# Performance work log

Hardware: AMD Instinct MI355X
Metric: run time of the kernel (lower is better)

The kernel has to match this reference:

```python
import jax, jax.numpy as jnp
import numpy as np

B, S, D, H, DFF = 2, 4096, 512, 8, 2048
DK = D // H
EPS = 1e-5


def layer_norm(x, g, b):
    mu = jnp.mean(x, axis=-1, keepdims=True)
    var = jnp.mean((x - mu) ** 2, axis=-1, keepdims=True)
    return (x - mu) * jax.lax.rsqrt(var + EPS) * g + b


def setup_inputs() -> dict:
    key = jax.random.key(0)
    ks = jax.random.split(key, 12)
    s = 1.0 / np.sqrt(D)
    return {
        "x": jax.random.normal(ks[0], (B, S, D), jnp.float32),
        "mask": jnp.ones((B, 1, 1, S), jnp.int32),
        "wq": jax.random.normal(ks[1], (D, D), jnp.float32) * s,
        "wk": jax.random.normal(ks[2], (D, D), jnp.float32) * s,
        "wv": jax.random.normal(ks[3], (D, D), jnp.float32) * s,
        "wo": jax.random.normal(ks[4], (D, D), jnp.float32) * s,
        "w1": jax.random.normal(ks[5], (D, DFF), jnp.float32) * s,
        "b1": jnp.zeros((DFF,), jnp.float32),
        "w2": jax.random.normal(ks[6], (DFF, D), jnp.float32) * (1.0 / np.sqrt(DFF)),
        "b2": jnp.zeros((D,), jnp.float32),
        "g1": jnp.ones((D,), jnp.float32),
        "be1": jnp.zeros((D,), jnp.float32),
        "g2": jnp.ones((D,), jnp.float32),
        "be2": jnp.zeros((D,), jnp.float32),
    }


def reference(x, mask, wq, wk, wv, wo, w1, b1, w2, b2, g1, be1, g2, be2):
    # projections -> [B, H, S, DK]
    def split_heads(t):
        return t.reshape(B, S, H, DK).transpose(0, 2, 1, 3)

    q = split_heads(x @ wq)
    k = split_heads(x @ wk)
    v = split_heads(x @ wv)

    scores = jnp.einsum("bhqd,bhkd->bhqk", q, k) / np.sqrt(DK)
    scores = jnp.where(mask == 0, -1e9, scores)
    attn = jax.nn.softmax(scores, axis=-1)  # dropout=0 (eval)
    ctx = jnp.einsum("bhqk,bhkd->bhqd", attn, v)
    ctx = ctx.transpose(0, 2, 1, 3).reshape(B, S, D)
    attn_out = ctx @ wo

    x1 = layer_norm(x + attn_out, g1, be1)
    ff = jax.nn.relu(x1 @ w1 + b1) @ w2 + b2
    return layer_norm(x1 + ff, g2, be2)
```

## Files before the change

### kernel.cpp

```cpp
#include <hip/hip_runtime.h>
#include <hip/hip_bf16.h>


typedef unsigned short u16;
typedef unsigned int u32;
typedef __attribute__((ext_vector_type(2))) u32 u32x2;
typedef __attribute__((ext_vector_type(4))) u16 u16x4;
typedef __attribute__((ext_vector_type(8))) u16 u16x8;
typedef __attribute__((ext_vector_type(2))) float f32x2;
typedef __attribute__((ext_vector_type(4))) float f32x4;
typedef __attribute__((ext_vector_type(16))) float f32x16;
typedef __attribute__((ext_vector_type(8))) short bf16x8;

#define CB 2
#define CS 4096
#define CD 512
#define CH 8
#define CDK 64
#define CDFF 2048
#define NXC ((size_t)CB * CS * CD)
#define NSP 2
#define BH (CB * CH)
#define BHS (BH * CS)

__device__ __forceinline__ float bf2f(u16 u) {
    union { u32 i; float f; } c;
    c.i = ((u32)u) << 16;
    return c.f;
}

__device__ __forceinline__ u16 f2bf(float f) {
    u32 x = __float_as_uint(f);
    u32 r = (x + 0x7fffu + ((x >> 16) & 1u)) >> 16;
    return (u16)r;
}

__device__ __forceinline__ u32 packbf2(float a, float b) {
    __hip_bfloat162 h = __float22bfloat162_rn(float2{a, b});
    union { __hip_bfloat162 h; u32 u; } c;
    c.h = h;
    return c.u;
}

__device__ __forceinline__ void dma16(const u16* g, u16* l) {
    __builtin_amdgcn_global_load_lds(
        (const __attribute__((address_space(1))) void*)g,
        (__attribute__((address_space(3))) void*)l, 16, 0, 0);
}

__global__ void detect_dtype(const u32* __restrict__ xw, int* __restrict__ flag) {
    __shared__ int red[256];
    int sane = 0;
    for (int i = threadIdx.x; i < 2048; i += 256) {
        u32 w = xw[i];
        u32 lo = w & 0xFFFFu;
        u32 e = (lo >> 7) & 0xFFu;
        if (lo == 0u || lo == 0x8000u || (e >= 96u && e <= 159u)) sane++;
    }
    red[threadIdx.x] = sane;
    __syncthreads();
    for (int s = 128; s > 0; s >>= 1) {
        if ((int)threadIdx.x < s) red[threadIdx.x] += red[threadIdx.x + s];
        __syncthreads();
    }
    if (threadIdx.x == 0) *flag = (red[0] >= 1843) ? 1 : 0;
}

__global__ __launch_bounds__(256) void convert_bf16(
    const void* __restrict__ src, u16* __restrict__ dst, int n,
    const int* __restrict__ flag)
{
    const bool isbf = (*flag != 0);
    const int n8 = n >> 3;
    int i = blockIdx.x * 256 + threadIdx.x;
    const int stride = gridDim.x * 256;
    if (isbf) {
        const u16x8* s = (const u16x8*)src;
        u16x8* d = (u16x8*)dst;
        for (; i < n8; i += stride) d[i] = s[i];
    } else {
        const f32x4* s = (const f32x4*)src;
        for (; i < n8; i += stride) {
            f32x4 a = s[2 * i];
            f32x4 b = s[2 * i + 1];
            u16x8 o;
#pragma unroll
            for (int e = 0; e < 4; e++) {
                o[e] = f2bf(a[e]);
                o[4 + e] = f2bf(b[e]);
            }
            *(u16x8*)&dst[(size_t)i * 8] = o;
        }
    }
    if (blockIdx.x == 0 && threadIdx.x == 0) {
        for (int r = n8 * 8; r < n; r++) {
            if (isbf) dst[r] = ((const u16*)src)[r];
            else dst[r] = f2bf(((const float*)src)[r]);
        }
    }
}

struct SmallConv {
    const void* src[6];
    u16* dst[6];
    int n[6];
};

__global__ __launch_bounds__(256) void convert_small(SmallConv sc, const int* __restrict__ flag) {
    const bool isbf = (*flag != 0);
    for (int t = 0; t < 6; t++) {
        for (int i = threadIdx.x; i < sc.n[t]; i += 256) {
            if (isbf) sc.dst[t][i] = ((const u16*)sc.src[t])[i];
            else sc.dst[t][i] = f2bf(((const float*)sc.src[t])[i]);
        }
    }
}

__global__ __launch_bounds__(256) void build_mask_bits(
    const int* __restrict__ mask, unsigned long long* __restrict__ bits)
{
    int w = blockIdx.x * 4 + (threadIdx.x >> 6);
    int lane = threadIdx.x & 63;
    int b = w >> 6, t = w & 63;
    int val = mask[b * CS + t * 64 + lane];
    unsigned long long bal = __ballot(val != 0);
    if (lane == 0) bits[w] = bal;
}

__global__ __launch_bounds__(256) void transpose_cvt(
    const void* __restrict__ src, u16* __restrict__ dst,
    int R, int Cc, const int* __restrict__ flag)
{
    __shared__ float t[32][33];
    const bool isbf = (*flag != 0);
    const int r0 = blockIdx.y * 32;
    const int c0 = blockIdx.x * 32;
    const int col = threadIdx.x & 31;
    const int row = threadIdx.x >> 5;
#pragma unroll
    for (int it = 0; it < 4; it++) {
        int rr = row + it * 8;
        float v;
        if (isbf) v = bf2f(((const u16*)src)[(size_t)(r0 + rr) * Cc + c0 + col]);
        else v = ((const float*)src)[(size_t)(r0 + rr) * Cc + c0 + col];
        t[rr][col] = v;
    }
    __syncthreads();
#pragma unroll
    for (int it = 0; it < 4; it++) {
        int rr = row + it * 8;
        dst[(size_t)(c0 + rr) * R + r0 + col] = f2bf(t[col][rr]);
    }
}

#define F_SPLIT 1
#define F_BIAS  2
#define F_RELU  4

template <int FLAGS>
__global__ __launch_bounds__(256, 2) void gemm_mfma(
    const u16* __restrict__ A, const u16* __restrict__ Bt,
    const u16* __restrict__ bias, u16* __restrict__ C,
    int M, int N, int K)
{
    __shared__ u16 Asb[4096];
    __shared__ u16 Bsb[4096];

    const int tid = threadIdx.x;
    const int lane = tid & 63;
    const int wave = tid >> 6;
    const int lrow = lane & 15;
    const int quad = lane >> 4;
    const int wm = wave & 1;
    const int wn = wave >> 1;
    const int m0 = blockIdx.y * 128;
    const int n0 = blockIdx.x * 128;

    const int idx0 = wave * 128 + lane;
    const int idx1 = idx0 + 64;
    const u16* Ap0 = A + (size_t)(m0 + (idx0 >> 2)) * K + (idx0 & 3) * 8;
    const u16* Ap1 = A + (size_t)(m0 + (idx1 >> 2)) * K + (idx1 & 3) * 8;
    const u16* Bp0 = Bt + (size_t)(n0 + (idx0 >> 2)) * K + (idx0 & 3) * 8;
    const u16* Bp1 = Bt + (size_t)(n0 + (idx1 >> 2)) * K + (idx1 & 3) * 8;
    u16* Al0 = &Asb[wave * 1024];
    u16* Al1 = &Asb[wave * 1024 + 512];
    u16* Bl0 = &Bsb[wave * 1024];
    u16* Bl1 = &Bsb[wave * 1024 + 512];

    f32x4 acc[4][4];
#pragma unroll
    for (int i = 0; i < 4; i++)
#pragma unroll
        for (int j = 0; j < 4; j++) acc[i][j] = f32x4{0.f, 0.f, 0.f, 0.f};

    for (int k0 = 0; k0 < K; k0 += 32) {
        __syncthreads();
        dma16(Ap0 + k0, Al0);
        dma16(Ap1 + k0, Al1);
        dma16(Bp0 + k0, Bl0);
        dma16(Bp1 + k0, Bl1);
        __syncthreads();

        bf16x8 af[4], bfr[4];
#pragma unroll
        for (int i = 0; i < 4; i++)
            af[i] = *(const bf16x8*)&Asb[(wm * 64 + i * 16 + lrow) * 32 + quad * 8];
#pragma unroll
        for (int j = 0; j < 4; j++)
            bfr[j] = *(const bf16x8*)&Bsb[(wn * 64 + j * 16 + lrow) * 32 + quad * 8];
#pragma unroll
        for (int i = 0; i < 4; i++)
#pragma unroll
            for (int j = 0; j < 4; j++)
                acc[i][j] = __builtin_amdgcn_mfma_f32_16x16x32_bf16(
                    af[i], bfr[j], acc[i][j], 0, 0, 0);
    }

    const int mbase = m0 + wm * 64;
    const int nbase = n0 + wn * 64;
#pragma unroll
    for (int i = 0; i < 4; i++) {
#pragma unroll
        for (int j = 0; j < 4; j++) {
            const int n = nbase + j * 16 + lrow;
            if ((FLAGS & F_SPLIT) && ((nbase + j * 16) >> 9) == 2) {
                const int dk = n & 63;
                const int h = (n >> 6) & 7;
                const int sb = mbase + i * 16 + quad * 4;
                const int bb = sb >> 12;
                const int ss = sb & 4095;
                u16x4 ov;
#pragma unroll
                for (int r = 0; r < 4; r++) ov[r] = f2bf(acc[i][j][r]);
                *(u16x4*)&C[2 * NXC + (((size_t)(bb * CH + h)) * CDK + dk) * CS + ss] = ov;
            } else {
#pragma unroll
                for (int r = 0; r < 4; r++) {
                    const int m = mbase + i * 16 + quad * 4 + r;
                    float val = acc[i][j][r];
                    if (FLAGS & F_BIAS) val += bf2f(bias[n]);
                    if (FLAGS & F_RELU) val = fmaxf(val, 0.f);
                    if (FLAGS & F_SPLIT) {
                        const int proj = n >> 9;
                        const int d = n & 511;
                        const int h = d >> 6;
                        const int dk = d & 63;
                        const int bb = m >> 12;
                        const int ss = m & 4095;
                        C[proj * NXC + (((size_t)(bb * CH + h)) * CS + ss) * CDK + dk] = f2bf(val);
                    } else {
                        C[(size_t)m * N + n] = f2bf(val);
                    }
                }
            }
        }
    }
}

__global__ __launch_bounds__(256, 4) void mfma_attn2(
    const u16* __restrict__ Qb, const u16* __restrict__ Kb,
    const u16* __restrict__ Vt, const unsigned long long* __restrict__ bits,
    u16* __restrict__ pOT, float* __restrict__ Ls)
{
    __shared__ u16 KB[3][4096];
    __shared__ u16 VB[2][4096];

    const int tid = threadIdx.x;
    const int lane = tid & 63;
    const int wave = tid >> 6;
    const int qcol = lane & 31;
    const int hf = lane >> 5;

    const int bh = blockIdx.y;
    const int b = bh >> 3;
    const int z = blockIdx.z;
    const int q0 = blockIdx.x * 128 + wave * 32;

    const float SC = 0.125f * 1.44269504088896340736f;

    bf16x8 bq[4];
    const u16* qp = Qb + ((size_t)bh * CS + q0 + qcol) * CDK + hf * 8;
#pragma unroll
    for (int c = 0; c < 4; c++) {
        bf16x8 raw = *(const bf16x8*)(qp + c * 16);
        union { u32 u[4]; bf16x8 v; } cv;
#pragma unroll
        for (int j = 0; j < 4; j++)
            cv.u[j] = packbf2(bf2f((u16)raw[2 * j]) * SC, bf2f((u16)raw[2 * j + 1]) * SC);
        bq[c] = cv.v;
    }

    f32x4 z4 = {0.f, 0.f, 0.f, 0.f};
    asm volatile("" : "+v"(z4));
    f32x16 zero16;
#pragma unroll
    for (int i = 0; i < 16; i++) zero16[i] = z4[i & 3];

    f32x16 ot[2];
#pragma unroll
    for (int dt = 0; dt < 2; dt++)
#pragma unroll
        for (int i = 0; i < 16; i++) ot[dt][i] = 0.f;
    float l = 0.f;

    const u16* kbase = Kb + (size_t)bh * CS * CDK;
    const u16* vbase = Vt + (size_t)bh * CDK * CS;
    const unsigned long long* bp = bits + b * 64;

    const int t0 = z * (CS / NSP);
    const int t1 = t0 + (CS / NSP);

    const int rsw = qcol & 7;
    int koff[2][4];
#pragma unroll
    for (int rt = 0; rt < 2; rt++)
#pragma unroll
        for (int c = 0; c < 4; c++)
            koff[rt][c] = ((rt * 32 + qcol) * 64 + (((2 * c + hf) ^ rsw) * 8)) * 2;
    const char* kb0 = (const char*)&KB[0][0];
    const char* vb0 = (const char*)&VB[0][0];

    const int w2 = wave * 2;

#define STAGE_K(KOFFB, t)                                                    \
    {                                                                        \
        const u16* kb_ = kbase + (size_t)(t) * CDK;                          \
        _Pragma("unroll")                                                    \
        for (int n = 0; n < 2; n++) {                                        \
            int idx = (w2 + n) * 64 + lane;                                  \
            int row = idx >> 3;                                              \
            int g = (idx & 7) ^ (row & 7);                                   \
            dma16(kb_ + row * CDK + g * 8,                                   \
                  (u16*)((char*)&KB[0][0] + (KOFFB) + (w2 + n) * 1024));     \
        }                                                                    \
    }
#define STAGE_V(P, t)                                                        \
    {                                                                        \
        const u16* vb_ = vbase + (t);                                        \
        _Pragma("unroll")                                                    \
        for (int n = 0; n < 2; n++) {                                        \
            int idx = (w2 + n) * 64 + lane;                                  \
            int row = idx >> 3;                                              \
            int g = (idx & 7) ^ (row & 7);                                   \
            dma16(vb_ + (size_t)row * CS + g * 8,                            \
                  (u16*)((char*)&VB[0][0] + (P) * 8192 + (w2 + n) * 1024));  \
        }                                                                    \
    }

#define TBODY(KROFF, VOFF, BM, MASKED, MIDSYNC)                              \
    {                                                                        \
        f32x2 racc = {0.f, 0.f};                                             \
        _Pragma("unroll")                                                    \
        for (int mt = 0; mt < 2; mt++) {                                     \
            f32x16 s;                                                        \
            _Pragma("unroll")                                                \
            for (int c = 0; c < 4; c++) {                                    \
                bf16x8 ak = *(const bf16x8*)(kb0 + (KROFF) + koff[mt][c]);   \
                s = __builtin_amdgcn_mfma_f32_32x32x16_bf16(                 \
                    ak, bq[c], (c == 0) ? zero16 : s, 0, 0, 0);              \
            }                                                                \
            if (MASKED) {                                                    \
                const unsigned long long bm_ = (BM);                         \
                if (bm_ != ~0ull) {                                          \
                    _Pragma("unroll")                                        \
                    for (int i = 0; i < 16; i++) {                           \
                        const int key = (i & 3) + 8 * (i >> 2) + 4 * hf + 32 * mt; \
                        if (!((bm_ >> key) & 1ull)) s[i] = -1e30f;           \
                    }                                                        \
                }                                                            \
            }                                                                \
            u32 pk[8];                                                       \
            _Pragma("unroll")                                                \
            for (int g = 0; g < 4; g++) {                                    \
                float p0 = __builtin_amdgcn_exp2f(s[4 * g + 0]);             \
                float p1 = __builtin_amdgcn_exp2f(s[4 * g + 1]);             \
                float p2 = __builtin_amdgcn_exp2f(s[4 * g + 2]);             \
                float p3 = __builtin_amdgcn_exp2f(s[4 * g + 3]);             \
                racc += f32x2{p0, p1};                                       \
                racc += f32x2{p2, p3};                                       \
                pk[2 * g + 0] = packbf2(p0, p1);                             \
                pk[2 * g + 1] = packbf2(p2, p3);                             \
            }                                                                \
            if (mt == 0) { MIDSYNC }                                         \
            _Pragma("unroll")                                                \
            for (int cc = 0; cc < 2; cc++) {                                 \
                u32x2 r0 = __builtin_amdgcn_permlane32_swap(                 \
                    pk[4 * cc + 0], pk[4 * cc + 2], false, false);           \
                u32x2 r1 = __builtin_amdgcn_permlane32_swap(                 \
                    pk[4 * cc + 1], pk[4 * cc + 3], false, false);           \
                union { u32 u[4]; bf16x8 v; } pf;                            \
                pf.u[0] = r0.x;                                              \
                pf.u[1] = r1.x;                                              \
                pf.u[2] = r0.y;                                              \
                pf.u[3] = r1.y;                                              \
                const int c = 2 * mt + cc;                                   \
                _Pragma("unroll")                                            \
                for (int dt = 0; dt < 2; dt++) {                             \
                    bf16x8 av = *(const bf16x8*)(vb0 + (VOFF) + koff[dt][c]); \
                    ot[dt] = __builtin_amdgcn_mfma_f32_32x32x16_bf16(        \
                        av, pf.v, ot[dt], 0, 0, 0);                          \
                }                                                            \
            }                                                                \
        }                                                                    \
        float rsv = racc.x + racc.y;                                         \
        u32x2 rr = __builtin_amdgcn_permlane32_swap(                         \
            __float_as_uint(rsv), __float_as_uint(rsv), false, false);       \
        l += rsv + __uint_as_float(hf ? rr.x : rr.y);                        \
    }

#define FTILE(P, TT, KR, KS, DOV, DOK, TOPASM, MIDASM)                       \
    {                                                                        \
        asm volatile(TOPASM ::: "memory");                                   \
        __builtin_amdgcn_sched_barrier(0);                                   \
        __builtin_amdgcn_s_barrier();                                        \
        __builtin_amdgcn_sched_barrier(0);                                   \
        if (DOV) STAGE_V((P) ^ 1, (TT) + 64);                                \
        if (DOK) STAGE_K((KS), (TT) + 128);                                  \
        TBODY((KR), (P) * 8192, 0ull, 0,                                     \
              asm volatile(MIDASM ::: "memory");                             \
              __builtin_amdgcn_sched_barrier(0);                             \
              __builtin_amdgcn_s_barrier();                                  \
              __builtin_amdgcn_sched_barrier(0);)                            \
    }

    unsigned long long am = ~0ull;
    const int tb0 = t0 >> 6;
    for (int i = 0; i < 32; i++) am &= bp[tb0 + i];
    const bool allones = (am == ~0ull);

    if (allones) {
        STAGE_K(0, t0);
        STAGE_V(0, t0);
        STAGE_K(8192, t0 + 64);

        u32 kr = 0;
        for (int m = 0; m < 15; m++) {
            const int t = t0 + m * 128;
            const u32 kr1 = (kr == 16384u) ? 0u : kr + 8192u;
            const u32 ks0 = (kr1 == 16384u) ? 0u : kr1 + 8192u;
            FTILE(0, t, kr, ks0, 1, 1,
                  "s_waitcnt vmcnt(4)", "s_waitcnt vmcnt(6)")
            FTILE(1, t + 64, kr1, kr, 1, 1,
                  "s_waitcnt vmcnt(4)", "s_waitcnt vmcnt(6)")
            kr = ks0;
        }
        {
            const int t = t0 + 30 * 64;
            const u32 kr1 = (kr == 16384u) ? 0u : kr + 8192u;
            FTILE(0, t, kr, 0, 1, 0,
                  "s_waitcnt vmcnt(4)", "s_waitcnt vmcnt(4)")
            FTILE(1, t + 64, kr1, 0, 0, 0,
                  "s_waitcnt vmcnt(2)", "s_waitcnt vmcnt(0)")
        }
    } else {
        STAGE_K(0, t0);
        STAGE_V(0, t0);
        __syncthreads();
        for (int t = t0; t < t1; t += 64) {
            const int p = (t >> 6) & 1;
            const u32 kro = (u32)p * 8192u;
            if (t + 64 < t1) {
                STAGE_V(p ^ 1, t + 64);
                STAGE_K((p ^ 1) * 8192, t + 64);
            }
            TBODY(kro, p * 8192, bp[t >> 6], 1, ;)
            __syncthreads();
        }
    }
#undef FTILE
#undef TBODY
#undef STAGE_V
#undef STAGE_K

    const int q_lin = bh * CS + q0 + qcol;
    if (hf == 0) Ls[z * BHS + q_lin] = l;
    const size_t pbase = ((size_t)(z * BH + bh) * CDK) * CS + q0 + qcol;
#pragma unroll
    for (int dt = 0; dt < 2; dt++)
#pragma unroll
        for (int i = 0; i < 16; i++) {
            const int dk = (i & 3) + 8 * (i >> 2) + 4 * hf + 32 * dt;
            pOT[pbase + (size_t)dk * CS] = f2bf(ot[dt][i]);
        }
}

__global__ __launch_bounds__(256) void attn_combine(
    const u16* __restrict__ pOT, const float* __restrict__ Ls,
    u16* __restrict__ ctx)
{
    __shared__ float linv[64];
    __shared__ u16 T[64][72];

    const int bh = blockIdx.y;
    const int s0 = blockIdx.x * 64;
    const int b = bh >> 3, h = bh & 7;
    const int tid = threadIdx.x;

    if (tid < 64) {
        float L = 0.f;
#pragma unroll
        for (int z = 0; z < NSP; z++) L += Ls[z * BHS + bh * CS + s0 + tid];
        linv[tid] = (L > 0.f) ? 1.f / L : 0.f;
    }
    __syncthreads();

    const int dk = tid >> 2;
    const int sc = (tid & 3) * 16;
    float acc[16] = {};
#pragma unroll
    for (int z = 0; z < NSP; z++) {
        const u16* p = pOT + ((size_t)(z * BH + bh) * CDK + dk) * CS + s0 + sc;
        u16x8 v0 = *(const u16x8*)p;
        u16x8 v1 = *(const u16x8*)(p + 8);
#pragma unroll
        for (int e = 0; e < 8; e++) {
            acc[e] += bf2f(v0[e]);
            acc[8 + e] += bf2f(v1[e]);
        }
    }
#pragma unroll
    for (int e = 0; e < 16; e++)
        T[sc + e][dk] = f2bf(acc[e] * linv[sc + e]);
    __syncthreads();

    const int sr = tid >> 2;
    const int dc = (tid & 3) * 16;
    u16x8 o0, o1;
#pragma unroll
    for (int e = 0; e < 8; e++) {
        o0[e] = T[sr][dc + e];
        o1[e] = T[sr][dc + 8 + e];
    }
    u16* cp = &ctx[((size_t)b * CS + s0 + sr) * CD + h * CDK + dc];
    *(u16x8*)cp = o0;
    *(u16x8*)(cp + 8) = o1;
}

__global__ __launch_bounds__(256) void ln_kernel(
    const u16* __restrict__ xa, const u16* __restrict__ xb,
    const u16* __restrict__ g, const u16* __restrict__ be,
    u16* __restrict__ outb, float* __restrict__ outf,
    const int* __restrict__ flag)
{
    const int lane = threadIdx.x & 63;
    const int wave = threadIdx.x >> 6;
    const size_t row = (size_t)blockIdx.x * 4 + wave;
    const int c0 = lane * 8;

    u16x8 av = *(const u16x8*)(xa + row * CD + c0);
    u16x8 bv = *(const u16x8*)(xb + row * CD + c0);

    float v[8];
    float s1 = 0.f, s2 = 0.f;
#pragma unroll
    for (int e = 0; e < 8; e++) {
        v[e] = bf2f(av[e]) + bf2f(bv[e]);
        s1 += v[e];
        s2 += v[e] * v[e];
    }
#pragma unroll
    for (int off = 32; off > 0; off >>= 1) {
        s1 += __shfl_xor(s1, off, 64);
        s2 += __shfl_xor(s2, off, 64);
    }
    const float mu = s1 * (1.f / CD);
    const float var = fmaxf(s2 * (1.f / CD) - mu * mu, 0.f);
    const float r = rsqrtf(var + 1e-5f);

    u16x8 gv = *(const u16x8*)(g + c0);
    u16x8 ev = *(const u16x8*)(be + c0);
    float res[8];
#pragma unroll
    for (int e = 0; e < 8; e++)
        res[e] = (v[e] - mu) * r * bf2f(gv[e]) + bf2f(ev[e]);

    const int flg = *flag;
    const bool f32out = (outf != nullptr) && (flg == 0);
    if (f32out) {
        float4 o0 = make_float4(res[0], res[1], res[2], res[3]);
        float4 o1 = make_float4(res[4], res[5], res[6], res[7]);
        *(float4*)(outf + row * CD + c0) = o0;
        *(float4*)(outf + row * CD + c0 + 4) = o1;
    } else {
        u16x8 ov;
#pragma unroll
        for (int e = 0; e < 8; e++) ov[e] = f2bf(res[e]);
        *(u16x8*)(outb + row * CD + c0) = ov;
    }
}


extern "C" void kernel_launch(void* const* d_in, const int* in_sizes, int n_in,
                              void* d_out, int out_size, void* d_ws, size_t ws_size,
                              hipStream_t stream)
{
    const void* x_raw   = d_in[0];
    const int*  mask    = (const int*)d_in[1];
    const void* wq_raw  = d_in[2];
    const void* wk_raw  = d_in[3];
    const void* wv_raw  = d_in[4];
    const void* wo_raw  = d_in[5];
    const void* w1_raw  = d_in[6];
    const void* b1_raw  = d_in[7];
    const void* w2_raw  = d_in[8];
    const void* b2_raw  = d_in[9];
    const void* g1_raw  = d_in[10];
    const void* be1_raw = d_in[11];
    const void* g2_raw  = d_in[12];
    const void* be2_raw = d_in[13];

    const size_t NX = NXC;
    const size_t WSZ = (size_t)CD * CD;
    const size_t W1SZ = (size_t)CD * CDFF;

    u16* ws = (u16*)d_ws;
    int* flag = (int*)d_ws;
    unsigned long long* bits = (unsigned long long*)(ws + 512);
    u16* base = ws + 1024;
    u16* xc  = base;
    u16* q   = base + 1 * NX;
    u16* k   = base + 2 * NX;
    u16* v   = base + 3 * NX;
    u16* ctx = base + 4 * NX;
    u16* att = base + 5 * NX;
    u16* x1  = base + 6 * NX;
    u16* ffo = base + 7 * NX;
    u16* ffh = base + 8 * NX;
    u16* wt  = base + 12 * NX;
    u16* wqkvT = wt;
    u16* woT = wqkvT + 3 * WSZ;
    u16* w1T = woT + WSZ;
    u16* w2T = w1T + W1SZ;
    u16* b1c = w2T + W1SZ;
    u16* b2c = b1c + CDFF;
    u16* g1c = b2c + CD;
    u16* be1c = g1c + CD;
    u16* g2c = be1c + CD;
    u16* be2c = g2c + CD;
    u16* wend = be2c + CD;

    const size_t need = (size_t)(wend - ws) * sizeof(u16);
    if (ws_size < need) return;
    (void)k;

    u16* pOT = ffh;
    float* Ls = (float*)att;

    detect_dtype<<<1, 256, 0, stream>>>((const u32*)x_raw, flag);

    convert_bf16<<<1024, 256, 0, stream>>>(x_raw, xc, (int)NX, flag);
    build_mask_bits<<<32, 256, 0, stream>>>(mask, bits);

    transpose_cvt<<<dim3(CD / 32, CD / 32), 256, 0, stream>>>(wq_raw, wqkvT, CD, CD, flag);
    transpose_cvt<<<dim3(CD / 32, CD / 32), 256, 0, stream>>>(wk_raw, wqkvT + WSZ, CD, CD, flag);
    transpose_cvt<<<dim3(CD / 32, CD / 32), 256, 0, stream>>>(wv_raw, wqkvT + 2 * WSZ, CD, CD, flag);
    transpose_cvt<<<dim3(CD / 32, CD / 32), 256, 0, stream>>>(wo_raw, woT, CD, CD, flag);
    transpose_cvt<<<dim3(CDFF / 32, CD / 32), 256, 0, stream>>>(w1_raw, w1T, CD, CDFF, flag);
    transpose_cvt<<<dim3(CD / 32, CDFF / 32), 256, 0, stream>>>(w2_raw, w2T, CDFF, CD, flag);

    SmallConv sc;
    sc.src[0] = b1_raw;  sc.dst[0] = b1c;  sc.n[0] = CDFF;
    sc.src[1] = b2_raw;  sc.dst[1] = b2c;  sc.n[1] = CD;
    sc.src[2] = g1_raw;  sc.dst[2] = g1c;  sc.n[2] = CD;
    sc.src[3] = be1_raw; sc.dst[3] = be1c; sc.n[3] = CD;
    sc.src[4] = g2_raw;  sc.dst[4] = g2c;  sc.n[4] = CD;
    sc.src[5] = be2_raw; sc.dst[5] = be2c; sc.n[5] = CD;
    convert_small<<<1, 256, 0, stream>>>(sc, flag);

    const int M = CB * CS;

    gemm_mfma<F_SPLIT><<<dim3(1536 / 128, M / 128), 256, 0, stream>>>(
        xc, wqkvT, nullptr, q, M, 1536, CD);

    mfma_attn2<<<dim3(CS / 128, BH, NSP), 256, 0, stream>>>(q, k, v, bits, pOT, Ls);
    attn_combine<<<dim3(CS / 64, BH), 256, 0, stream>>>(pOT, Ls, ctx);

    gemm_mfma<0><<<dim3(CD / 128, M / 128), 256, 0, stream>>>(
        ctx, woT, nullptr, att, M, CD, CD);

    ln_kernel<<<dim3(M / 4), 256, 0, stream>>>(xc, att, g1c, be1c, x1, nullptr, flag);

    gemm_mfma<F_BIAS | F_RELU><<<dim3(CDFF / 128, M / 128), 256, 0, stream>>>(
        x1, w1T, b1c, ffh, M, CDFF, CD);
    gemm_mfma<F_BIAS><<<dim3(CD / 128, M / 128), 256, 0, stream>>>(
        ffh, w2T, b2c, ffo, M, CD, CDFF);

    ln_kernel<<<dim3(M / 4), 256, 0, stream>>>(x1, ffo, g2c, be2c,
                                               (u16*)d_out, (float*)d_out, flag);
}
```

Before: 339.9 us.

## Drop mid-tile barrier, unroll K ring by six, defer row-sum lane swap

Removes the second workgroup barrier and its vmcnt wait inside each attention tile, leaving one barrier per tile. The fast path is unrolled six tiles deep so the three-slot K ring and two-slot V ring offsets become compile-time constants, replacing the runtime modulo arithmetic. The per-tile permlane32 swap used for the softmax row sum is moved to a single swap after the loop. Taking out the mid-tile barrier relies on the remaining top barrier and wait count being enough to protect the K and V buffers from being overwritten while still in use, so there is some risk of a race on shared memory.

```diff
diff --git a/kernel.cpp b/kernel.cpp
--- a/kernel.cpp
+++ b/kernel.cpp
@@ -301,7 +301,7 @@
     for (int dt = 0; dt < 2; dt++)
 #pragma unroll
         for (int i = 0; i < 16; i++) ot[dt][i] = 0.f;
-    float l = 0.f;
+    float lh = 0.f;
 
     const u16* kbase = Kb + (size_t)bh * CS * CDK;
     const u16* vbase = Vt + (size_t)bh * CDK * CS;
@@ -347,7 +347,7 @@
         }                                                                    \
     }
 
-#define TBODY(KROFF, VOFF, BM, MASKED, MIDSYNC)                              \
+#define TBODY(KROFF, VOFF, BM, MASKED)                                       \
     {                                                                        \
         f32x2 racc = {0.f, 0.f};                                             \
         _Pragma("unroll")                                                    \
@@ -381,7 +381,6 @@
                 pk[2 * g + 0] = packbf2(p0, p1);                             \
                 pk[2 * g + 1] = packbf2(p2, p3);                             \
             }                                                                \
-            if (mt == 0) { MIDSYNC }                                         \
             _Pragma("unroll")                                                \
             for (int cc = 0; cc < 2; cc++) {                                 \
                 u32x2 r0 = __builtin_amdgcn_permlane32_swap(                 \
@@ -402,25 +401,18 @@
                 }                                                            \
             }                                                                \
         }                                                                    \
-        float rsv = racc.x + racc.y;                                         \
-        u32x2 rr = __builtin_amdgcn_permlane32_swap(                         \
-            __float_as_uint(rsv), __float_as_uint(rsv), false, false);       \
-        l += rsv + __uint_as_float(hf ? rr.x : rr.y);                        \
-    }
-
-#define FTILE(P, TT, KR, KS, DOV, DOK, TOPASM, MIDASM)                       \
+        lh += racc.x + racc.y;                                               \
+    }
+
+#define FTILE(P, KR, TT, DOV, DOK, KS, WAITASM)                              \
     {                                                                        \
-        asm volatile(TOPASM ::: "memory");                                   \
+        asm volatile(WAITASM ::: "memory");                                  \
         __builtin_amdgcn_sched_barrier(0);                                   \
         __builtin_amdgcn_s_barrier();                                        \
         __builtin_amdgcn_sched_barrier(0);                                   \
         if (DOV) STAGE_V((P) ^ 1, (TT) + 64);                                \
         if (DOK) STAGE_K((KS), (TT) + 128);                                  \
-        TBODY((KR), (P) * 8192, 0ull, 0,                                     \
-              asm volatile(MIDASM ::: "memory");                             \
-              __builtin_amdgcn_sched_barrier(0);                             \
-              __builtin_amdgcn_s_barrier();                                  \
-              __builtin_amdgcn_sched_barrier(0);)                            \
+        TBODY((KR), (P) * 8192, 0ull, 0)                                     \
     }
 
     unsigned long long am = ~0ull;
@@ -433,25 +425,17 @@
         STAGE_V(0, t0);
         STAGE_K(8192, t0 + 64);
 
-        u32 kr = 0;
-        for (int m = 0; m < 15; m++) {
-            const int t = t0 + m * 128;
-            const u32 kr1 = (kr == 16384u) ? 0u : kr + 8192u;
-            const u32 ks0 = (kr1 == 16384u) ? 0u : kr1 + 8192u;
-            FTILE(0, t, kr, ks0, 1, 1,
-                  "s_waitcnt vmcnt(4)", "s_waitcnt vmcnt(6)")
-            FTILE(1, t + 64, kr1, kr, 1, 1,
-                  "s_waitcnt vmcnt(4)", "s_waitcnt vmcnt(6)")
-            kr = ks0;
-        }
-        {
-            const int t = t0 + 30 * 64;
-            const u32 kr1 = (kr == 16384u) ? 0u : kr + 8192u;
-            FTILE(0, t, kr, 0, 1, 0,
-                  "s_waitcnt vmcnt(4)", "s_waitcnt vmcnt(4)")
-            FTILE(1, t + 64, kr1, 0, 0, 0,
-                  "s_waitcnt vmcnt(2)", "s_waitcnt vmcnt(0)")
-        }
+        for (int m = 0; m < 5; m++) {
+            const int t = t0 + m * 384;
+            FTILE(0, 0,     t,       1, 1, 16384, "s_waitcnt vmcnt(2)")
+            FTILE(1, 8192,  t + 64,  1, 1, 0,     "s_waitcnt vmcnt(2)")
+            FTILE(0, 16384, t + 128, 1, 1, 8192,  "s_waitcnt vmcnt(2)")
+            FTILE(1, 0,     t + 192, 1, 1, 16384, "s_waitcnt vmcnt(2)")
+            FTILE(0, 8192,  t + 256, 1, 1, 0,     "s_waitcnt vmcnt(2)")
+            FTILE(1, 16384, t + 320, 1, 1, 8192,  "s_waitcnt vmcnt(2)")
+        }
+        FTILE(0, 0, t0 + 1920, 1, 0, 0, "s_waitcnt vmcnt(2)")
+        FTILE(1, 8192, t0 + 1984, 0, 0, 0, "s_waitcnt vmcnt(0)")
     } else {
         STAGE_K(0, t0);
         STAGE_V(0, t0);
@@ -463,7 +447,7 @@
                 STAGE_V(p ^ 1, t + 64);
                 STAGE_K((p ^ 1) * 8192, t + 64);
             }
-            TBODY(kro, p * 8192, bp[t >> 6], 1, ;)
+            TBODY(kro, p * 8192, bp[t >> 6], 1)
             __syncthreads();
         }
     }
@@ -471,6 +455,10 @@
 #undef TBODY
 #undef STAGE_V
 #undef STAGE_K
+
+    u32x2 rr = __builtin_amdgcn_permlane32_swap(
+        __float_as_uint(lh), __float_as_uint(lh), false, false);
+    const float l = lh + __uint_as_float(hf ? rr.x : rr.y);
 
     const int q_lin = bh * CS + q0 + qcol;
     if (hf == 0) Ls[z * BHS + q_lin] = l;
```

After: 353.3 us. 3.9% more time.

## Triple-buffer GEMM LDS staging and defer attention row-sum lane swap

Applied to the files above, without the earlier changes.

The bf16 MFMA GEMM now keeps three LDS buffers and issues asynchronous global-to-LDS loads two k-steps ahead. Each step uses an explicit vmcnt wait and a single barrier, replacing the two full barriers per k-step that left load latency exposed. A fallback loop handles K values that do not fit the unrolled schedule. In the attention kernel, the per-tile permlane32 swap for the softmax row sum is moved out of the loop and done once at the end. The cost is triple the GEMM shared memory (48KB), which may reduce occupancy under launch_bounds(256,2).

```diff
diff --git a/kernel.cpp b/kernel.cpp
--- a/kernel.cpp
+++ b/kernel.cpp
@@ -163,8 +163,8 @@
     const u16* __restrict__ bias, u16* __restrict__ C,
     int M, int N, int K)
 {
-    __shared__ u16 Asb[4096];
-    __shared__ u16 Bsb[4096];
+    __shared__ u16 AS[3][4096];
+    __shared__ u16 BS[3][4096];
 
     const int tid = threadIdx.x;
     const int lane = tid & 63;
@@ -182,10 +182,6 @@
     const u16* Ap1 = A + (size_t)(m0 + (idx1 >> 2)) * K + (idx1 & 3) * 8;
     const u16* Bp0 = Bt + (size_t)(n0 + (idx0 >> 2)) * K + (idx0 & 3) * 8;
     const u16* Bp1 = Bt + (size_t)(n0 + (idx1 >> 2)) * K + (idx1 & 3) * 8;
-    u16* Al0 = &Asb[wave * 1024];
-    u16* Al1 = &Asb[wave * 1024 + 512];
-    u16* Bl0 = &Bsb[wave * 1024];
-    u16* Bl1 = &Bsb[wave * 1024 + 512];
 
     f32x4 acc[4][4];
 #pragma unroll
@@ -193,28 +189,66 @@
 #pragma unroll
         for (int j = 0; j < 4; j++) acc[i][j] = f32x4{0.f, 0.f, 0.f, 0.f};
 
-    for (int k0 = 0; k0 < K; k0 += 32) {
-        __syncthreads();
-        dma16(Ap0 + k0, Al0);
-        dma16(Ap1 + k0, Al1);
-        dma16(Bp0 + k0, Bl0);
-        dma16(Bp1 + k0, Bl1);
-        __syncthreads();
-
-        bf16x8 af[4], bfr[4];
-#pragma unroll
-        for (int i = 0; i < 4; i++)
-            af[i] = *(const bf16x8*)&Asb[(wm * 64 + i * 16 + lrow) * 32 + quad * 8];
-#pragma unroll
-        for (int j = 0; j < 4; j++)
-            bfr[j] = *(const bf16x8*)&Bsb[(wn * 64 + j * 16 + lrow) * 32 + quad * 8];
-#pragma unroll
-        for (int i = 0; i < 4; i++)
-#pragma unroll
-            for (int j = 0; j < 4; j++)
-                acc[i][j] = __builtin_amdgcn_mfma_f32_16x16x32_bf16(
-                    af[i], bfr[j], acc[i][j], 0, 0, 0);
-    }
+#define GSTAGE(B, KOFF)                                                      \
+    {                                                                        \
+        dma16(Ap0 + (KOFF), &AS[B][wave * 1024]);                            \
+        dma16(Ap1 + (KOFF), &AS[B][wave * 1024 + 512]);                      \
+        dma16(Bp0 + (KOFF), &BS[B][wave * 1024]);                            \
+        dma16(Bp1 + (KOFF), &BS[B][wave * 1024 + 512]);                      \
+    }
+#define GCOMP(B)                                                             \
+    {                                                                        \
+        bf16x8 af[4], bfr[4];                                                \
+        _Pragma("unroll")                                                    \
+        for (int i = 0; i < 4; i++)                                          \
+            af[i] = *(const bf16x8*)&AS[B][(wm * 64 + i * 16 + lrow) * 32 + quad * 8]; \
+        _Pragma("unroll")                                                    \
+        for (int j = 0; j < 4; j++)                                          \
+            bfr[j] = *(const bf16x8*)&BS[B][(wn * 64 + j * 16 + lrow) * 32 + quad * 8]; \
+        _Pragma("unroll")                                                    \
+        for (int i = 0; i < 4; i++)                                          \
+            _Pragma("unroll")                                                \
+            for (int j = 0; j < 4; j++)                                      \
+                acc[i][j] = __builtin_amdgcn_mfma_f32_16x16x32_bf16(         \
+                    af[i], bfr[j], acc[i][j], 0, 0, 0);                      \
+    }
+#define GITER(B, KOFF, DOS, SB, SKOFF, WAIT)                                 \
+    {                                                                        \
+        asm volatile(WAIT ::: "memory");                                     \
+        __builtin_amdgcn_sched_barrier(0);                                   \
+        __builtin_amdgcn_s_barrier();                                        \
+        __builtin_amdgcn_sched_barrier(0);                                   \
+        if (DOS) GSTAGE(SB, SKOFF);                                          \
+        GCOMP(B)                                                             \
+    }
+
+    const int NK = K >> 5;
+    if (NK >= 7 && ((NK - 4) % 3) == 0) {
+        GSTAGE(0, 0);
+        GSTAGE(1, 32);
+        int kk = 0;
+        const int MCH = (NK - 4) / 3;
+        for (int m = 0; m < MCH; m++) {
+            GITER(0, kk,      1, 2, kk + 64,  "s_waitcnt vmcnt(4)")
+            GITER(1, kk + 32, 1, 0, kk + 96,  "s_waitcnt vmcnt(4)")
+            GITER(2, kk + 64, 1, 1, kk + 128, "s_waitcnt vmcnt(4)")
+            kk += 96;
+        }
+        GITER(0, kk,      1, 2, kk + 64, "s_waitcnt vmcnt(4)")
+        GITER(1, kk + 32, 1, 0, kk + 96, "s_waitcnt vmcnt(4)")
+        GITER(2, kk + 64, 0, 0, 0,       "s_waitcnt vmcnt(4)")
+        GITER(0, kk + 96, 0, 0, 0,       "s_waitcnt vmcnt(0)")
+    } else {
+        for (int k0 = 0; k0 < K; k0 += 32) {
+            __syncthreads();
+            GSTAGE(0, k0);
+            __syncthreads();
+            GCOMP(0)
+        }
+    }
+#undef GITER
+#undef GCOMP
+#undef GSTAGE
 
     const int mbase = m0 + wm * 64;
     const int nbase = n0 + wn * 64;
@@ -301,7 +335,7 @@
     for (int dt = 0; dt < 2; dt++)
 #pragma unroll
         for (int i = 0; i < 16; i++) ot[dt][i] = 0.f;
-    float l = 0.f;
+    float lh = 0.f;
 
     const u16* kbase = Kb + (size_t)bh * CS * CDK;
     const u16* vbase = Vt + (size_t)bh * CDK * CS;
@@ -402,10 +436,7 @@
                 }                                                            \
             }                                                                \
         }                                                                    \
-        float rsv = racc.x + racc.y;                                         \
-        u32x2 rr = __builtin_amdgcn_permlane32_swap(                         \
-            __float_as_uint(rsv), __float_as_uint(rsv), false, false);       \
-        l += rsv + __uint_as_float(hf ? rr.x : rr.y);                        \
+        lh += racc.x + racc.y;                                               \
     }
 
 #define FTILE(P, TT, KR, KS, DOV, DOK, TOPASM, MIDASM)                       \
@@ -471,6 +502,10 @@
 #undef TBODY
 #undef STAGE_V
 #undef STAGE_K
+
+    u32x2 rr = __builtin_amdgcn_permlane32_swap(
+        __float_as_uint(lh), __float_as_uint(lh), false, false);
+    const float l = lh + __uint_as_float(hf ? rr.x : rr.y);
 
     const int q_lin = bh * CS + q0 + qcol;
     if (hf == 0) Ls[z * BHS + q_lin] = l;
```

Result: slower. 359.0 us (+5.6%).
